# Optimization experiments

Measured on AMD Instinct MI355X. Metric: run time of the kernel, lower is better.

The kernel has to match this reference:

```python
import jax, jax.numpy as jnp
import numpy as np

ALPHA = 0.2        # LeakyReLU slope
NEG_BIG = -9e15    # mask fill value from the original module


def setup_inputs() -> dict:
    key = jax.random.key(0)
    k1, k2, k3, k4 = jax.random.split(key, 4)
    N, F_IN, F_OUT = 8192, 256, 128
    h = jax.random.normal(k1, (N, F_IN), dtype=jnp.float32)
    adj = jax.random.randint(k2, (N, N), 0, 2, dtype=jnp.int32)
    W = jax.random.normal(k3, (F_IN, F_OUT), dtype=jnp.float32) * (1.0 / np.sqrt(F_IN))
    a = jax.random.normal(k4, (2 * F_OUT, 1), dtype=jnp.float32) * (1.0 / np.sqrt(2 * F_OUT))
    return {"h": h, "adj": adj, "W": W, "a": a}


def reference(h, adj, W, a):
    f_out = W.shape[1]
    Wh = h @ W                                   # [N, F_out]
    Wh1 = Wh @ a[:f_out, :]                      # [N, 1]
    Wh2 = Wh @ a[f_out:, :]                      # [N, 1]
    e = Wh1 + Wh2.T                              # [N, N] broadcast-add
    e = jnp.where(e > 0, e, ALPHA * e)           # LeakyReLU
    e = jnp.where(adj > 0, e, NEG_BIG)           # adjacency mask
    attention = jax.nn.softmax(e, axis=-1)       # row softmax
    # dropout rate = 0.0 -> identity
    h_prime = attention @ Wh                     # [N, F_out]
    return jax.nn.elu(h_prime)
```

## Files before the change

### kernel.cpp

```cpp
#include <hip/hip_runtime.h>

#define NV 8192
#define FIN 256
#define FOUT 128

typedef __bf16 bf16_t;
typedef __attribute__((ext_vector_type(8))) __bf16 bf16x8;
typedef __attribute__((ext_vector_type(16))) float f32x16;

__global__ __launch_bounds__(256) void wh_kernel(
    const float* __restrict__ h, const float* __restrict__ W,
    const float* __restrict__ a,
    bf16_t* __restrict__ WhbT, float* __restrict__ Wh1, float* __restrict__ Wh2)
{
  __shared__ float As[64][34];
  __shared__ float Bs[64][128];
  __shared__ float Cs[32][129];
  __shared__ float red1[32][16];
  __shared__ float red2[32][16];
  const int t  = threadIdx.x;
  const int i0 = blockIdx.x * 32;
  const int c  = t & 15;
  const int r  = t >> 4;
  float acc0[8], acc1[8];
  #pragma unroll
  for (int j = 0; j < 8; j++) { acc0[j] = 0.f; acc1[j] = 0.f; }

  for (int k0 = 0; k0 < FIN; k0 += 64) {
    {
      const int ia = t >> 3;
      const int ka = (t & 7) * 8;
      const float* src = h + (size_t)(i0 + ia) * FIN + k0 + ka;
      float4 v0 = *(const float4*)src;
      float4 v1 = *(const float4*)(src + 4);
      As[ka+0][ia]=v0.x; As[ka+1][ia]=v0.y; As[ka+2][ia]=v0.z; As[ka+3][ia]=v0.w;
      As[ka+4][ia]=v1.x; As[ka+5][ia]=v1.y; As[ka+6][ia]=v1.z; As[ka+7][ia]=v1.w;
    }
    {
      const int kb = t >> 2;
      const int cb = (t & 3) * 32;
      const float4* src = (const float4*)(W + (size_t)(k0 + kb) * FOUT + cb);
      float4* dst = (float4*)&Bs[kb][cb];
      #pragma unroll
      for (int q = 0; q < 8; q++) dst[q] = src[q];
    }
    __syncthreads();
    #pragma unroll 4
    for (int k = 0; k < 64; k++) {
      float2 av = *(const float2*)&As[k][r*2];
      float b[8];
      *(float4*)&b[0] = *(const float4*)&Bs[k][c*8];
      *(float4*)&b[4] = *(const float4*)&Bs[k][c*8+4];
      #pragma unroll
      for (int j = 0; j < 8; j++) {
        acc0[j] = fmaf(av.x, b[j], acc0[j]);
        acc1[j] = fmaf(av.y, b[j], acc1[j]);
      }
    }
    __syncthreads();
  }

  float p1a = 0.f, p2a = 0.f, p1b = 0.f, p2b = 0.f;
  #pragma unroll
  for (int j = 0; j < 8; j++) {
    Cs[r*2][c*8+j]   = acc0[j];
    Cs[r*2+1][c*8+j] = acc1[j];
    float w1 = a[c*8+j];
    float w2 = a[FOUT + c*8+j];
    p1a = fmaf(acc0[j], w1, p1a); p2a = fmaf(acc0[j], w2, p2a);
    p1b = fmaf(acc1[j], w1, p1b); p2b = fmaf(acc1[j], w2, p2b);
  }
  red1[r*2][c]   = p1a; red2[r*2][c]   = p2a;
  red1[r*2+1][c] = p1b; red2[r*2+1][c] = p2b;
  __syncthreads();
  if (t < 32) {
    float s = 0.f;
    #pragma unroll
    for (int q = 0; q < 16; q++) s += red1[t][q];
    Wh1[i0 + t] = s;
  } else if (t < 64) {
    float s = 0.f;
    #pragma unroll
    for (int q = 0; q < 16; q++) s += red2[t-32][q];
    Wh2[i0 + t - 32] = s;
  }
  {
    const int f = t & 127, half = t >> 7;
    union { bf16_t b[16]; uint4 v[2]; } pk;
    #pragma unroll
    for (int q = 0; q < 16; q++) pk.b[q] = (bf16_t)Cs[half*16 + q][f];
    uint4* dst = (uint4*)(WhbT + (size_t)f * NV + i0 + half*16);
    dst[0] = pk.v[0]; dst[1] = pk.v[1];
  }
}

__global__ __launch_bounds__(256) void attn_kernel(
    const int* __restrict__ adj, const bf16_t* __restrict__ WhbT,
    const float* __restrict__ Wh1v, const float* __restrict__ Wh2v,
    float* __restrict__ nump, float* __restrict__ denp)
{
  __shared__ bf16_t Plds[64][72];
  __shared__ bf16_t Blds[128][72];
  __shared__ float denlds[64][4];
  const int t     = threadIdx.x;
  const int rb    = blockIdx.x >> 2;
  const int split = blockIdx.x & 3;
  const int i0 = rb * 64;
  const int j0 = split * 2048;
  const int il = t >> 2;
  const int jg = (t & 3) * 16;
  const float wh1 = Wh1v[i0 + il];
  const int lane = t & 63;
  const int w    = t >> 6;
  const int rh = (w & 1) * 32;
  const int ch = (w >> 1) * 64;
  const int ml = lane & 31;
  const int kh = (lane >> 5) * 8;
  f32x16 acc0 = {};
  f32x16 acc1 = {};
  float den_t = 0.f;

  for (int jc = 0; jc < 2048; jc += 64) {
    const int jb = j0 + jc;
    __syncthreads();
    {
      const int n  = t >> 1;
      const int hf = (t & 1) * 32;
      const uint4* s4 = (const uint4*)(WhbT + (size_t)n * NV + jb + hf);
      uint4* dst = (uint4*)&Blds[n][hf];
      dst[0] = s4[0]; dst[1] = s4[1]; dst[2] = s4[2]; dst[3] = s4[3];
    }
    {
      const int* arow = adj + (size_t)(i0 + il) * NV + jb + jg;
      int4 a0 = *(const int4*)arow;
      int4 a1 = *(const int4*)(arow + 4);
      int4 a2 = *(const int4*)(arow + 8);
      int4 a3 = *(const int4*)(arow + 12);
      float4 w0 = *(const float4*)(Wh2v + jb + jg);
      float4 w1 = *(const float4*)(Wh2v + jb + jg + 4);
      float4 w2 = *(const float4*)(Wh2v + jb + jg + 8);
      float4 w3 = *(const float4*)(Wh2v + jb + jg + 12);
      const int am[16] = {a0.x,a0.y,a0.z,a0.w, a1.x,a1.y,a1.z,a1.w,
                          a2.x,a2.y,a2.z,a2.w, a3.x,a3.y,a3.z,a3.w};
      const float wm[16] = {w0.x,w0.y,w0.z,w0.w, w1.x,w1.y,w1.z,w1.w,
                            w2.x,w2.y,w2.z,w2.w, w3.x,w3.y,w3.z,w3.w};
      bf16x8 pv0, pv1;
      #pragma unroll
      for (int q = 0; q < 16; q++) {
        float e = wh1 + wm[q];
        e = fmaxf(e, 0.2f * e);
        float p = (am[q] > 0) ? __expf(e) : 0.0f;
        den_t += p;
        if (q < 8) pv0[q] = (bf16_t)p; else pv1[q-8] = (bf16_t)p;
      }
      *(bf16x8*)&Plds[il][jg]     = pv0;
      *(bf16x8*)&Plds[il][jg + 8] = pv1;
    }
    __syncthreads();
    #pragma unroll
    for (int ks = 0; ks < 4; ks++) {
      const int k = ks * 16 + kh;
      bf16x8 af = *(const bf16x8*)&Plds[rh + ml][k];
      bf16x8 b0 = *(const bf16x8*)&Blds[ch + ml][k];
      bf16x8 b1 = *(const bf16x8*)&Blds[ch + 32 + ml][k];
      acc0 = __builtin_amdgcn_mfma_f32_32x32x16_bf16(af, b0, acc0, 0, 0, 0);
      acc1 = __builtin_amdgcn_mfma_f32_32x32x16_bf16(af, b1, acc1, 0, 0, 0);
    }
  }

  denlds[il][t & 3] = den_t;
  __syncthreads();
  if (t < 64) {
    denp[(size_t)split * NV + i0 + t] =
        denlds[t][0] + denlds[t][1] + denlds[t][2] + denlds[t][3];
  }
  float* base = nump + ((size_t)split * NV + i0) * FOUT;
  const int col = ch + ml;
  const int r4  = 4 * (lane >> 5);
  #pragma unroll
  for (int reg = 0; reg < 16; reg++) {
    const int row = rh + (reg & 3) + 8 * (reg >> 2) + r4;
    base[(size_t)row * FOUT + col]      = acc0[reg];
    base[(size_t)row * FOUT + col + 32] = acc1[reg];
  }
}

__global__ __launch_bounds__(256) void finalize_kernel(
    const float* __restrict__ nump, const float* __restrict__ denp,
    float* __restrict__ out)
{
  const int gid = blockIdx.x * 256 + threadIdx.x;
  const int i  = gid >> 5;
  const int f0 = (gid & 31) * 4;
  const float den = denp[i] + denp[NV + i] + denp[2*NV + i] + denp[3*NV + i];
  float4 s = make_float4(0.f, 0.f, 0.f, 0.f);
  #pragma unroll
  for (int sp = 0; sp < 4; sp++) {
    float4 v = *(const float4*)&nump[((size_t)sp * NV + i) * FOUT + f0];
    s.x += v.x; s.y += v.y; s.z += v.z; s.w += v.w;
  }
  const float inv = 1.0f / den;
  float4 r;
  r.x = s.x * inv; r.y = s.y * inv; r.z = s.z * inv; r.w = s.w * inv;
  r.x = r.x > 0.f ? r.x : __expf(r.x) - 1.0f;
  r.y = r.y > 0.f ? r.y : __expf(r.y) - 1.0f;
  r.z = r.z > 0.f ? r.z : __expf(r.z) - 1.0f;
  r.w = r.w > 0.f ? r.w : __expf(r.w) - 1.0f;
  *(float4*)&out[(size_t)i * FOUT + f0] = r;
}

extern "C" void kernel_launch(void* const* d_in, const int* in_sizes, int n_in,
                              void* d_out, int out_size, void* d_ws, size_t ws_size,
                              hipStream_t stream) {
  const float* h  = (const float*)d_in[0];
  const int*  adj = (const int*)d_in[1];
  const float* W  = (const float*)d_in[2];
  const float* a  = (const float*)d_in[3];
  float* out = (float*)d_out;
  char* ws = (char*)d_ws;
  bf16_t* WhbT = (bf16_t*)ws;
  float* Wh1  = (float*)(ws + 2097152);
  float* Wh2  = (float*)(ws + 2097152 + 32768);
  float* denp = (float*)(ws + 2097152 + 65536);
  float* nump = (float*)(ws + 2097152 + 65536 + 131072);

  wh_kernel<<<256, 256, 0, stream>>>(h, W, a, WhbT, Wh1, Wh2);
  attn_kernel<<<512, 256, 0, stream>>>(adj, WhbT, Wh1, Wh2, nump, denp);
  finalize_kernel<<<1024, 256, 0, stream>>>(nump, denp, out);
}
```

Baseline: 415.0 us.

## Split attention columns eight ways and prefetch adjacency rows one chunk ahead

Doubles the column split of the attention kernel from four to eight, launching twice as many blocks to fill more compute units, and asks for three blocks per SIMD via launch bounds. Adjacency loads for the next 64-column chunk are issued before the current chunk is processed, so global latency overlaps the exp and MFMA work. The barrier is rearranged into a raw LDS wait plus barrier. The cost is twice the partial numerator and denominator traffic for the finalize kernel to reduce, and more register pressure from the prefetch buffers.

```diff
diff --git a/kernel.cpp b/kernel.cpp
--- a/kernel.cpp
+++ b/kernel.cpp
@@ -3,6 +3,8 @@
 #define NV 8192
 #define FIN 256
 #define FOUT 128
+#define NSPLIT 8
+#define SPLITW 1024
 
 typedef __bf16 bf16_t;
 typedef __attribute__((ext_vector_type(8))) __bf16 bf16x8;
@@ -94,7 +96,7 @@
   }
 }
 
-__global__ __launch_bounds__(256) void attn_kernel(
+__global__ __launch_bounds__(256, 3) void attn_kernel(
     const int* __restrict__ adj, const bf16_t* __restrict__ WhbT,
     const float* __restrict__ Wh1v, const float* __restrict__ Wh2v,
     float* __restrict__ nump, float* __restrict__ denp)
@@ -103,10 +105,10 @@
   __shared__ bf16_t Blds[128][72];
   __shared__ float denlds[64][4];
   const int t     = threadIdx.x;
-  const int rb    = blockIdx.x >> 2;
-  const int split = blockIdx.x & 3;
+  const int rb    = blockIdx.x >> 3;
+  const int split = blockIdx.x & 7;
   const int i0 = rb * 64;
-  const int j0 = split * 2048;
+  const int j0 = split * SPLITW;
   const int il = t >> 2;
   const int jg = (t & 3) * 16;
   const float wh1 = Wh1v[i0 + il];
@@ -120,9 +122,20 @@
   f32x16 acc1 = {};
   float den_t = 0.f;
 
-  for (int jc = 0; jc < 2048; jc += 64) {
+  const int* arow = adj + (size_t)(i0 + il) * NV + j0 + jg;
+  int4 ca0 = *(const int4*)(arow + 0);
+  int4 ca1 = *(const int4*)(arow + 4);
+  int4 ca2 = *(const int4*)(arow + 8);
+  int4 ca3 = *(const int4*)(arow + 12);
+
+  for (int jc = 0; jc < SPLITW; jc += 64) {
     const int jb = j0 + jc;
-    __syncthreads();
+    const int jn = (jc + 64 < SPLITW) ? jc + 64 : jc;
+    const int* nrow = arow + jn;
+    int4 na0 = *(const int4*)(nrow + 0);
+    int4 na1 = *(const int4*)(nrow + 4);
+    int4 na2 = *(const int4*)(nrow + 8);
+    int4 na3 = *(const int4*)(nrow + 12);
     {
       const int n  = t >> 1;
       const int hf = (t & 1) * 32;
@@ -131,17 +144,12 @@
       dst[0] = s4[0]; dst[1] = s4[1]; dst[2] = s4[2]; dst[3] = s4[3];
     }
     {
-      const int* arow = adj + (size_t)(i0 + il) * NV + jb + jg;
-      int4 a0 = *(const int4*)arow;
-      int4 a1 = *(const int4*)(arow + 4);
-      int4 a2 = *(const int4*)(arow + 8);
-      int4 a3 = *(const int4*)(arow + 12);
       float4 w0 = *(const float4*)(Wh2v + jb + jg);
       float4 w1 = *(const float4*)(Wh2v + jb + jg + 4);
       float4 w2 = *(const float4*)(Wh2v + jb + jg + 8);
       float4 w3 = *(const float4*)(Wh2v + jb + jg + 12);
-      const int am[16] = {a0.x,a0.y,a0.z,a0.w, a1.x,a1.y,a1.z,a1.w,
-                          a2.x,a2.y,a2.z,a2.w, a3.x,a3.y,a3.z,a3.w};
+      const int am[16] = {ca0.x,ca0.y,ca0.z,ca0.w, ca1.x,ca1.y,ca1.z,ca1.w,
+                          ca2.x,ca2.y,ca2.z,ca2.w, ca3.x,ca3.y,ca3.z,ca3.w};
       const float wm[16] = {w0.x,w0.y,w0.z,w0.w, w1.x,w1.y,w1.z,w1.w,
                             w2.x,w2.y,w2.z,w2.w, w3.x,w3.y,w3.z,w3.w};
       bf16x8 pv0, pv1;
@@ -156,7 +164,7 @@
       *(bf16x8*)&Plds[il][jg]     = pv0;
       *(bf16x8*)&Plds[il][jg + 8] = pv1;
     }
-    __syncthreads();
+    asm volatile("s_waitcnt lgkmcnt(0)\n\ts_barrier" ::: "memory");
     #pragma unroll
     for (int ks = 0; ks < 4; ks++) {
       const int k = ks * 16 + kh;
@@ -166,6 +174,8 @@
       acc0 = __builtin_amdgcn_mfma_f32_32x32x16_bf16(af, b0, acc0, 0, 0, 0);
       acc1 = __builtin_amdgcn_mfma_f32_32x32x16_bf16(af, b1, acc1, 0, 0, 0);
     }
+    __syncthreads();
+    ca0 = na0; ca1 = na1; ca2 = na2; ca3 = na3;
   }
 
   denlds[il][t & 3] = den_t;
@@ -192,10 +202,12 @@
   const int gid = blockIdx.x * 256 + threadIdx.x;
   const int i  = gid >> 5;
   const int f0 = (gid & 31) * 4;
-  const float den = denp[i] + denp[NV + i] + denp[2*NV + i] + denp[3*NV + i];
+  float den = 0.f;
+  #pragma unroll
+  for (int sp = 0; sp < NSPLIT; sp++) den += denp[(size_t)sp * NV + i];
   float4 s = make_float4(0.f, 0.f, 0.f, 0.f);
   #pragma unroll
-  for (int sp = 0; sp < 4; sp++) {
+  for (int sp = 0; sp < NSPLIT; sp++) {
     float4 v = *(const float4*)&nump[((size_t)sp * NV + i) * FOUT + f0];
     s.x += v.x; s.y += v.y; s.z += v.z; s.w += v.w;
   }
@@ -222,9 +234,9 @@
   float* Wh1  = (float*)(ws + 2097152);
   float* Wh2  = (float*)(ws + 2097152 + 32768);
   float* denp = (float*)(ws + 2097152 + 65536);
-  float* nump = (float*)(ws + 2097152 + 65536 + 131072);
+  float* nump = (float*)(ws + 2097152 + 65536 + 262144);
 
   wh_kernel<<<256, 256, 0, stream>>>(h, W, a, WhbT, Wh1, Wh2);
-  attn_kernel<<<512, 256, 0, stream>>>(adj, WhbT, Wh1, Wh2, nump, denp);
+  attn_kernel<<<1024, 256, 0, stream>>>(adj, WhbT, Wh1, Wh2, nump, denp);
   finalize_kernel<<<1024, 256, 0, stream>>>(nump, denp, out);
 }
```

Measured after the change: 412.3 us. About the same (-0.6%).
